# Optimization experiments

Measured on AMD Instinct MI355X. Metric: run time of the kernel, lower is better.

Reference implementation:

```python
import jax, jax.numpy as jnp
import numpy as np

IN_F = 4096
OUT_F = 4096
RANK = 16
ALPHA = 32
BLOCK = 64  # quantization blocksize along in_features
SCALING = ALPHA / RANK


def setup_inputs() -> dict:
    key = jax.random.key(0)
    k1, k2, k3, k4, k5, k6 = jax.random.split(key, 6)
    x = jax.random.normal(k1, (4, 2048, IN_F), dtype=jnp.float32)
    # int4 codes stored with +8 offset, values in [0, 16)
    q_codes = jax.random.randint(k2, (OUT_F, IN_F), 0, 16, dtype=jnp.int32)
    # per-(row, block) dequant scales
    scales = jax.random.uniform(k3, (OUT_F, IN_F // BLOCK), dtype=jnp.float32) * 0.02
    bias = jax.random.normal(k4, (OUT_F,), dtype=jnp.float32) * 0.02
    lora_A = jax.random.normal(k5, (RANK, IN_F), dtype=jnp.float32) * (1.0 / np.sqrt(IN_F))
    lora_B = jax.random.normal(k6, (OUT_F, RANK), dtype=jnp.float32) * 0.02
    return {"x": x, "q_codes": q_codes, "scales": scales, "bias": bias,
            "lora_A": lora_A, "lora_B": lora_B}


def _dequant(q_codes, scales):
    # [O, I] int4 codes (offset by 8) -> fp32 weight via blockwise scales
    O, I = q_codes.shape
    c = (q_codes.astype(jnp.float32) - 8.0).reshape(O, I // BLOCK, BLOCK)
    return (c * scales[:, :, None]).reshape(O, I)


def reference(x, q_codes, scales, bias, lora_A, lora_B):
    w = _dequant(q_codes, scales)                      # [O, I]
    base = jnp.einsum('bsi,oi->bso', x, w) + bias      # dequant GEMM + bias
    # LoRA branch: dropout(p=0) is identity; x @ (B@A).T == (x @ A.T) @ B.T
    lora = jnp.einsum('bsr,or->bso', jnp.einsum('bsi,ri->bsr', x, lora_A), lora_B)
    return base + lora * SCALING
```

## Files before the change

### kernel.cpp

```cpp
#include <hip/hip_runtime.h>
#include <hip/hip_bf16.h>

#define IN_F   4096
#define OUT_F  4096
#define RANK   16
#define M_TOK  8192
#define SCALING 2.0f

typedef __attribute__((ext_vector_type(8))) short short8;
typedef __attribute__((ext_vector_type(4))) float f32x4;
typedef __attribute__((ext_vector_type(4))) float fvec4;
typedef __attribute__((ext_vector_type(4))) int   ivec4;
typedef __attribute__((ext_vector_type(4))) unsigned int uvec4;

__global__ __launch_bounds__(256) void cvt_x(const float* __restrict__ x,
                                             __hip_bfloat16* __restrict__ xb) {
    const size_t nvec = (size_t)M_TOK * IN_F / 8;
    const size_t stride = (size_t)gridDim.x * 256;
    for (size_t idx = (size_t)blockIdx.x * 256 + threadIdx.x; idx < nvec; idx += stride) {
        const size_t i = idx * 8;
        fvec4 a = __builtin_nontemporal_load((const fvec4*)(x + i));
        fvec4 b = __builtin_nontemporal_load((const fvec4*)(x + i + 4));
        union { uvec4 u; __hip_bfloat16 h[8]; } p;
        p.h[0] = __float2bfloat16(a.x);
        p.h[1] = __float2bfloat16(a.y);
        p.h[2] = __float2bfloat16(a.z);
        p.h[3] = __float2bfloat16(a.w);
        p.h[4] = __float2bfloat16(b.x);
        p.h[5] = __float2bfloat16(b.y);
        p.h[6] = __float2bfloat16(b.z);
        p.h[7] = __float2bfloat16(b.w);
        *(uvec4*)(xb + i) = p.u;
    }
}

__global__ __launch_bounds__(256) void dequant_lora(const int* __restrict__ q,
                                                    const float* __restrict__ sc,
                                                    const float* __restrict__ lA,
                                                    const float* __restrict__ lB,
                                                    __hip_bfloat16* __restrict__ W) {
    const int tid = threadIdx.x;
    const int id  = blockIdx.x;
    const int c0  = (id & 3) * 1024 + tid * 4;
    const int o0  = (id >> 2) * 8;

    ivec4 qv[8];
#pragma unroll
    for (int oo = 0; oo < 8; ++oo)
        qv[oo] = __builtin_nontemporal_load(
            (const ivec4*)(q + (size_t)(o0 + oo) * IN_F + c0));

    float sv[8];
#pragma unroll
    for (int oo = 0; oo < 8; ++oo)
        sv[oo] = sc[(o0 + oo) * (IN_F / 64) + (c0 >> 6)];

    fvec4 a[RANK];
#pragma unroll
    for (int r = 0; r < RANK; ++r)
        a[r] = *(const fvec4*)(lA + (size_t)r * IN_F + c0);

#pragma unroll
    for (int oo = 0; oo < 8; ++oo) {
        const float* lbo = lB + (size_t)(o0 + oo) * RANK;
        float l0 = 0.f, l1 = 0.f, l2 = 0.f, l3 = 0.f;
#pragma unroll
        for (int r = 0; r < RANK; ++r) {
            const float br = lbo[r];
            l0 += br * a[r].x; l1 += br * a[r].y;
            l2 += br * a[r].z; l3 += br * a[r].w;
        }
        const float s = sv[oo];
        union { ushort4 u; __hip_bfloat16 h[4]; } p;
        p.h[0] = __float2bfloat16((float)(qv[oo].x - 8) * s + SCALING * l0);
        p.h[1] = __float2bfloat16((float)(qv[oo].y - 8) * s + SCALING * l1);
        p.h[2] = __float2bfloat16((float)(qv[oo].z - 8) * s + SCALING * l2);
        p.h[3] = __float2bfloat16((float)(qv[oo].w - 8) * s + SCALING * l3);
        *(ushort4*)(W + (size_t)(o0 + oo) * IN_F + c0) = p.u;
    }
}


__device__ __forceinline__ void load_lds16(const void* g, void* l) {
    __builtin_amdgcn_global_load_lds(
        (const __attribute__((address_space(1))) unsigned int*)g,
        (__attribute__((address_space(3))) unsigned int*)l, 16, 0, 0);
}

#define MFMA_BF16 __builtin_amdgcn_mfma_f32_16x16x32_bf16

__global__ __launch_bounds__(512, 2) void gemm256_8ph(const __hip_bfloat16* __restrict__ A,
                                                      const __hip_bfloat16* __restrict__ B,
                                                      const float* __restrict__ bias,
                                                      float* __restrict__ C) {
    extern __shared__ __align__(16) char lds[];

    const int tid  = threadIdx.x;
    const int lane = tid & 63;
    const int wave = tid >> 6;

    const int xcd = blockIdx.x & 7;
    const int w64 = blockIdx.x >> 3;
    const int tm  = (xcd >> 1) * 8 + (w64 >> 3);
    const int tn  = (xcd & 1) * 8 + (w64 & 7);

    const __hip_bfloat16* Ab = A + (size_t)tm * 256 * IN_F;
    const __hip_bfloat16* Bb = B + (size_t)tn * 256 * IN_F;

    const int    c0   = ((lane & 3) * 8) ^ ((lane >= 32) ? 16 : 0);
    const size_t off0 = (size_t)((wave >> 1) * 16 + (lane >> 2)) * IN_F
                      + (size_t)((wave & 1) * 32 + c0);

    const __hip_bfloat16* qA0 = Ab + off0;
    const __hip_bfloat16* qA1 = Ab + (size_t)128 * IN_F + off0;
    const __hip_bfloat16* qB0 = Bb + off0;
    const __hip_bfloat16* qB1 = Bb + (size_t)128 * IN_F + off0;

    const int flo = (lane & 15) * 64 + (((lane >> 4) * 16) ^ ((lane & 8) << 2));

    const int ah = wave >> 2;
    const int bh = (wave >> 1) & 1;
    const int bs = (wave & 1) * 4;

    const char* aRd[2] = { lds + ah * 16384 + flo,
                           lds + 65536 + ah * 16384 + flo };
    const char* bRd[2] = { lds + 32768 + bh * 16384 + bs * 2048 + flo,
                           lds + 65536 + 32768 + bh * 16384 + bs * 2048 + flo };

    const int wv1024 = wave * 1024;

#define STAGE2(ps, te, LO) do {                                             \
        const __hip_bfloat16* g_ = (ps) + (te);                             \
        load_lds16(g_,              lds + (LO) + wv1024);                   \
        load_lds16(g_ + 64 * IN_F,  lds + (LO) + 8192 + wv1024);            \
    } while (0)

    STAGE2(qB0, 0,  32768);
    STAGE2(qB1, 0,  49152);
    STAGE2(qA0, 0,  0);
    STAGE2(qA1, 0,  16384);
    STAGE2(qB0, 64, 65536 + 32768);
    STAGE2(qB1, 64, 65536 + 49152);
    asm volatile("s_waitcnt vmcnt(4)" ::: "memory");
    __builtin_amdgcn_s_barrier();

    short8 aF[4][2], bAf[2][2], bBf[2][2];
    f32x4 acc[8][4] = {};

#define TILE(T, CBI) do {                                                          \
        const int t1e = (((T) + 1) & 63) << 6;        \
        const int t2e = (((T) + 2) & 63) << 6;                                     \
                           \
        _Pragma("unroll")                                                          \
        for (int i = 0; i < 4; ++i)                                                \
            _Pragma("unroll")                                                      \
            for (int kk = 0; kk < 2; ++kk)                                         \
                aF[i][kk] = *(const short8*)(aRd[CBI] + (i * 2 + kk) * 1024);      \
        _Pragma("unroll")                                                          \
        for (int j = 0; j < 2; ++j)                                                \
            _Pragma("unroll")                                                      \
            for (int kk = 0; kk < 2; ++kk)                                         \
                bAf[j][kk] = *(const short8*)(bRd[CBI] + (j * 2 + kk) * 1024);     \
        STAGE2(qA0, t1e, ((CBI) ^ 1) * 65536);                                     \
        __builtin_amdgcn_s_barrier();                                              \
        __builtin_amdgcn_s_setprio(1);                                             \
        _Pragma("unroll")                                                          \
        for (int i = 0; i < 4; ++i)                                                \
            _Pragma("unroll")                                                      \
            for (int j = 0; j < 2; ++j)                                            \
                _Pragma("unroll")                                                  \
                for (int kk = 0; kk < 2; ++kk)                                     \
                    acc[i][j] = MFMA_BF16(aF[i][kk], bAf[j][kk], acc[i][j], 0,0,0);\
        __builtin_amdgcn_s_setprio(0);                                             \
        __builtin_amdgcn_s_barrier();                                              \
                           \
        _Pragma("unroll")                                                          \
        for (int j = 0; j < 2; ++j)                                                \
            _Pragma("unroll")                                                      \
            for (int kk = 0; kk < 2; ++kk)                                         \
                bBf[j][kk] = *(const short8*)(bRd[CBI] + 4096 + (j*2+kk) * 1024);  \
        STAGE2(qA1, t1e, ((CBI) ^ 1) * 65536 + 16384);                             \
        __builtin_amdgcn_s_barrier();                                              \
        __builtin_amdgcn_s_setprio(1);                                             \
        _Pragma("unroll")                                                          \
        for (int i = 0; i < 4; ++i)                                                \
            _Pragma("unroll")                                                      \
            for (int j = 0; j < 2; ++j)                                            \
                _Pragma("unroll")                                                  \
                for (int kk = 0; kk < 2; ++kk)                                     \
                    acc[i][2+j] = MFMA_BF16(aF[i][kk], bBf[j][kk], acc[i][2+j],0,0,0);\
        __builtin_amdgcn_s_setprio(0);                                             \
        __builtin_amdgcn_s_barrier();                                              \
                           \
        _Pragma("unroll")                                                          \
        for (int i = 0; i < 4; ++i)                                                \
            _Pragma("unroll")                                                      \
            for (int kk = 0; kk < 2; ++kk)                                         \
                aF[i][kk] = *(const short8*)(aRd[CBI] + 8192 + (i*2+kk) * 1024);   \
        STAGE2(qB0, t2e, (CBI) * 65536 + 32768);               \
        __builtin_amdgcn_s_barrier();                                              \
        __builtin_amdgcn_s_setprio(1);                                             \
        _Pragma("unroll")                                                          \
        for (int i = 0; i < 4; ++i)                                                \
            _Pragma("unroll")                                                      \
            for (int j = 0; j < 2; ++j)                                            \
                _Pragma("unroll")                                                  \
                for (int kk = 0; kk < 2; ++kk)                                     \
                    acc[4+i][2+j] = MFMA_BF16(aF[i][kk], bBf[j][kk], acc[4+i][2+j],0,0,0);\
        __builtin_amdgcn_s_setprio(0);                                             \
        __builtin_amdgcn_s_barrier();                                              \
                           \
        STAGE2(qB1, t2e, (CBI) * 65536 + 49152);                                   \
        asm volatile("s_waitcnt vmcnt(4)" ::: "memory");      \
        __builtin_amdgcn_s_barrier();                          \
        __builtin_amdgcn_s_setprio(1);                                             \
        _Pragma("unroll")                                                          \
        for (int i = 0; i < 4; ++i)                                                \
            _Pragma("unroll")                                                      \
            for (int j = 0; j < 2; ++j)                                            \
                _Pragma("unroll")                                                  \
                for (int kk = 0; kk < 2; ++kk)                                     \
                    acc[4+i][j] = MFMA_BF16(aF[i][kk], bAf[j][kk], acc[4+i][j],0,0,0);\
        __builtin_amdgcn_s_setprio(0);                                             \
        __builtin_amdgcn_s_barrier();                                              \
    } while (0)

    for (int tt = 0; tt < 32; ++tt) {
        TILE(2 * tt,     0);
        TILE(2 * tt + 1, 1);
    }
    asm volatile("s_waitcnt vmcnt(0)" ::: "memory");

    const int qd = lane >> 4;
    const int cl = lane & 15;
    const size_t m_base = (size_t)tm * 256 + (size_t)ah * 128;
    const int    n_base = tn * 256 + (wave & 3) * 64;
#pragma unroll
    for (int fn = 0; fn < 4; ++fn) {
        const int n = n_base + fn * 16 + cl;
        const float bv = bias[n];
#pragma unroll
        for (int fm = 0; fm < 8; ++fm) {
            const size_t m0 = m_base + fm * 16 + qd * 4;
#pragma unroll
            for (int r = 0; r < 4; ++r)
                __builtin_nontemporal_store(acc[fm][fn][r] + bv,
                                            &C[(m0 + r) * OUT_F + n]);
        }
    }
#undef STAGE2
#undef TILE
}

extern "C" void kernel_launch(void* const* d_in, const int* in_sizes, int n_in,
                              void* d_out, int out_size, void* d_ws, size_t ws_size,
                              hipStream_t stream) {
    const float* x    = (const float*)d_in[0];
    const int*   qc   = (const int*)d_in[1];
    const float* sc   = (const float*)d_in[2];
    const float* bias = (const float*)d_in[3];
    const float* lA   = (const float*)d_in[4];
    const float* lB   = (const float*)d_in[5];
    float* out = (float*)d_out;

    __hip_bfloat16* xb = (__hip_bfloat16*)d_ws;
    __hip_bfloat16* wb = xb + (size_t)M_TOK * IN_F;

    static bool attr_done = false;
    if (!attr_done) {
        (void)hipFuncSetAttribute((const void*)gemm256_8ph,
                                  hipFuncAttributeMaxDynamicSharedMemorySize, 131072);
        attr_done = true;
    }

    cvt_x<<<2048, 256, 0, stream>>>(x, xb);
    dequant_lora<<<2048, 256, 0, stream>>>(qc, sc, lA, lB, wb);
    gemm256_8ph<<<dim3(512), dim3(512), 131072, stream>>>(xb, wb, bias, out);
}
```

Measured before the change: 481.6 us.

## Switch GEMM core to 32x32x16 bf16 MFMA with matching LDS layout

Replaces the 16x16x32 MFMA tiling with 32x32x16 MFMA instructions, reorganising per-wave fragments into 2x2 blocks of 32x32 accumulators. The global-to-LDS staging layout and the LDS read addressing change to a plain 32-row layout without the previous XOR swizzle, and the epilogue is rewritten for the 32x32 output layout. The aim is fewer MFMA issues and fewer LDS fragment reads per tile. The cost is a risk of LDS bank conflicts now that the swizzle is gone.

New measurement: 505.7 us. 5.0% more time.

```diff
diff --git a/kernel.cpp b/kernel.cpp
--- a/kernel.cpp
+++ b/kernel.cpp
@@ -7,11 +7,12 @@
 #define M_TOK  8192
 #define SCALING 2.0f
 
-typedef __attribute__((ext_vector_type(8))) short short8;
-typedef __attribute__((ext_vector_type(4))) float f32x4;
-typedef __attribute__((ext_vector_type(4))) float fvec4;
-typedef __attribute__((ext_vector_type(4))) int   ivec4;
-typedef __attribute__((ext_vector_type(4))) unsigned int uvec4;
+typedef __attribute__((ext_vector_type(8)))  short short8;
+typedef __attribute__((ext_vector_type(4)))  float f32x4;
+typedef __attribute__((ext_vector_type(16))) float f32x16;
+typedef __attribute__((ext_vector_type(4)))  float fvec4;
+typedef __attribute__((ext_vector_type(4)))  int   ivec4;
+typedef __attribute__((ext_vector_type(4)))  unsigned int uvec4;
 
 __global__ __launch_bounds__(256) void cvt_x(const float* __restrict__ x,
                                              __hip_bfloat16* __restrict__ xb) {
@@ -87,7 +88,7 @@
         (__attribute__((address_space(3))) unsigned int*)l, 16, 0, 0);
 }
 
-#define MFMA_BF16 __builtin_amdgcn_mfma_f32_16x16x32_bf16
+#define MFMA32 __builtin_amdgcn_mfma_f32_32x32x16_bf16
 
 __global__ __launch_bounds__(512, 2) void gemm256_8ph(const __hip_bfloat16* __restrict__ A,
                                                       const __hip_bfloat16* __restrict__ B,
@@ -107,25 +108,23 @@
     const __hip_bfloat16* Ab = A + (size_t)tm * 256 * IN_F;
     const __hip_bfloat16* Bb = B + (size_t)tn * 256 * IN_F;
 
-    const int    c0   = ((lane & 3) * 8) ^ ((lane >= 32) ? 16 : 0);
-    const size_t off0 = (size_t)((wave >> 1) * 16 + (lane >> 2)) * IN_F
-                      + (size_t)((wave & 1) * 32 + c0);
+    const size_t off0 = (size_t)((wave >> 2) * 32 + (lane >> 1)) * IN_F
+                      + (size_t)((wave & 3) * 16 + (lane & 1) * 8);
 
     const __hip_bfloat16* qA0 = Ab + off0;
     const __hip_bfloat16* qA1 = Ab + (size_t)128 * IN_F + off0;
     const __hip_bfloat16* qB0 = Bb + off0;
     const __hip_bfloat16* qB1 = Bb + (size_t)128 * IN_F + off0;
 
-    const int flo = (lane & 15) * 64 + (((lane >> 4) * 16) ^ ((lane & 8) << 2));
+    const int lrd = (lane & 31) * 32 + (lane >> 5) * 16;
 
     const int ah = wave >> 2;
     const int bh = (wave >> 1) & 1;
-    const int bs = (wave & 1) * 4;
-
-    const char* aRd[2] = { lds + ah * 16384 + flo,
-                           lds + 65536 + ah * 16384 + flo };
-    const char* bRd[2] = { lds + 32768 + bh * 16384 + bs * 2048 + flo,
-                           lds + 65536 + 32768 + bh * 16384 + bs * 2048 + flo };
+
+    const char* aRd[2] = { lds + ah * 16384 + lrd,
+                           lds + 65536 + ah * 16384 + lrd };
+    const char* bRd[2] = { lds + 32768 + bh * 16384 + (wave & 1) * 8192 + lrd,
+                           lds + 65536 + 32768 + bh * 16384 + (wave & 1) * 8192 + lrd };
 
     const int wv1024 = wave * 1024;
 
@@ -144,83 +143,71 @@
     asm volatile("s_waitcnt vmcnt(4)" ::: "memory");
     __builtin_amdgcn_s_barrier();
 
-    short8 aF[4][2], bAf[2][2], bBf[2][2];
-    f32x4 acc[8][4] = {};
+    short8 aF[2][4], bA[4], bB[4];
+    f32x16 acc[4][2] = {};
 
 #define TILE(T, CBI) do {                                                          \
         const int t1e = (((T) + 1) & 63) << 6;        \
         const int t2e = (((T) + 2) & 63) << 6;                                     \
-                           \
-        _Pragma("unroll")                                                          \
-        for (int i = 0; i < 4; ++i)                                                \
+                          \
+        _Pragma("unroll")                                                          \
+        for (int i = 0; i < 2; ++i)                                                \
             _Pragma("unroll")                                                      \
-            for (int kk = 0; kk < 2; ++kk)                                         \
-                aF[i][kk] = *(const short8*)(aRd[CBI] + (i * 2 + kk) * 1024);      \
-        _Pragma("unroll")                                                          \
-        for (int j = 0; j < 2; ++j)                                                \
+            for (int ks = 0; ks < 4; ++ks)                                         \
+                aF[i][ks] = *(const short8*)(aRd[CBI] + (i * 4 + ks) * 1024);      \
+        _Pragma("unroll")                                                          \
+        for (int ks = 0; ks < 4; ++ks)                                             \
+            bA[ks] = *(const short8*)(bRd[CBI] + ks * 1024);                       \
+        STAGE2(qA0, t1e, ((CBI) ^ 1) * 65536);                                     \
+        __builtin_amdgcn_s_barrier();                                              \
+        __builtin_amdgcn_s_setprio(1);                                             \
+        _Pragma("unroll")                                                          \
+        for (int ks = 0; ks < 4; ++ks) {                                           \
+            acc[0][0] = MFMA32(aF[0][ks], bA[ks], acc[0][0], 0, 0, 0);             \
+            acc[1][0] = MFMA32(aF[1][ks], bA[ks], acc[1][0], 0, 0, 0);             \
+        }                                                                          \
+        __builtin_amdgcn_s_setprio(0);                                             \
+        __builtin_amdgcn_s_barrier();                                              \
+                          \
+        _Pragma("unroll")                                                          \
+        for (int ks = 0; ks < 4; ++ks)                                             \
+            bB[ks] = *(const short8*)(bRd[CBI] + 4096 + ks * 1024);                \
+        STAGE2(qA1, t1e, ((CBI) ^ 1) * 65536 + 16384);                             \
+        __builtin_amdgcn_s_barrier();                                              \
+        __builtin_amdgcn_s_setprio(1);                                             \
+        _Pragma("unroll")                                                          \
+        for (int ks = 0; ks < 4; ++ks) {                                           \
+            acc[0][1] = MFMA32(aF[0][ks], bB[ks], acc[0][1], 0, 0, 0);             \
+            acc[1][1] = MFMA32(aF[1][ks], bB[ks], acc[1][1], 0, 0, 0);             \
+        }                                                                          \
+        __builtin_amdgcn_s_setprio(0);                                             \
+        __builtin_amdgcn_s_barrier();                                              \
+                          \
+        _Pragma("unroll")                                                          \
+        for (int i = 0; i < 2; ++i)                                                \
             _Pragma("unroll")                                                      \
-            for (int kk = 0; kk < 2; ++kk)                                         \
-                bAf[j][kk] = *(const short8*)(bRd[CBI] + (j * 2 + kk) * 1024);     \
-        STAGE2(qA0, t1e, ((CBI) ^ 1) * 65536);                                     \
-        __builtin_amdgcn_s_barrier();                                              \
-        __builtin_amdgcn_s_setprio(1);                                             \
-        _Pragma("unroll")                                                          \
-        for (int i = 0; i < 4; ++i)                                                \
-            _Pragma("unroll")                                                      \
-            for (int j = 0; j < 2; ++j)                                            \
-                _Pragma("unroll")                                                  \
-                for (int kk = 0; kk < 2; ++kk)                                     \
-                    acc[i][j] = MFMA_BF16(aF[i][kk], bAf[j][kk], acc[i][j], 0,0,0);\
-        __builtin_amdgcn_s_setprio(0);                                             \
-        __builtin_amdgcn_s_barrier();                                              \
-                           \
-        _Pragma("unroll")                                                          \
-        for (int j = 0; j < 2; ++j)                                                \
-            _Pragma("unroll")                                                      \
-            for (int kk = 0; kk < 2; ++kk)                                         \
-                bBf[j][kk] = *(const short8*)(bRd[CBI] + 4096 + (j*2+kk) * 1024);  \
-        STAGE2(qA1, t1e, ((CBI) ^ 1) * 65536 + 16384);                             \
-        __builtin_amdgcn_s_barrier();                                              \
-        __builtin_amdgcn_s_setprio(1);                                             \
-        _Pragma("unroll")                                                          \
-        for (int i = 0; i < 4; ++i)                                                \
-            _Pragma("unroll")                                                      \
-            for (int j = 0; j < 2; ++j)                                            \
-                _Pragma("unroll")                                                  \
-                for (int kk = 0; kk < 2; ++kk)                                     \
-                    acc[i][2+j] = MFMA_BF16(aF[i][kk], bBf[j][kk], acc[i][2+j],0,0,0);\
-        __builtin_amdgcn_s_setprio(0);                                             \
-        __builtin_amdgcn_s_barrier();                                              \
-                           \
-        _Pragma("unroll")                                                          \
-        for (int i = 0; i < 4; ++i)                                                \
-            _Pragma("unroll")                                                      \
-            for (int kk = 0; kk < 2; ++kk)                                         \
-                aF[i][kk] = *(const short8*)(aRd[CBI] + 8192 + (i*2+kk) * 1024);   \
-        STAGE2(qB0, t2e, (CBI) * 65536 + 32768);               \
-        __builtin_amdgcn_s_barrier();                                              \
-        __builtin_amdgcn_s_setprio(1);                                             \
-        _Pragma("unroll")                                                          \
-        for (int i = 0; i < 4; ++i)                                                \
-            _Pragma("unroll")                                                      \
-            for (int j = 0; j < 2; ++j)                                            \
-                _Pragma("unroll")                                                  \
-                for (int kk = 0; kk < 2; ++kk)                                     \
-                    acc[4+i][2+j] = MFMA_BF16(aF[i][kk], bBf[j][kk], acc[4+i][2+j],0,0,0);\
-        __builtin_amdgcn_s_setprio(0);                                             \
-        __builtin_amdgcn_s_barrier();                                              \
-                           \
+            for (int ks = 0; ks < 4; ++ks)                                         \
+                aF[i][ks] = *(const short8*)(aRd[CBI] + 8192 + (i * 4 + ks) * 1024);\
+        STAGE2(qB0, t2e, (CBI) * 65536 + 32768);         \
+        __builtin_amdgcn_s_barrier();                                              \
+        __builtin_amdgcn_s_setprio(1);                                             \
+        _Pragma("unroll")                                                          \
+        for (int ks = 0; ks < 4; ++ks) {                                           \
+            acc[2][1] = MFMA32(aF[0][ks], bB[ks], acc[2][1], 0, 0, 0);             \
+            acc[3][1] = MFMA32(aF[1][ks], bB[ks], acc[3][1], 0, 0, 0);             \
+        }                                                                          \
+        __builtin_amdgcn_s_setprio(0);                                             \
+        __builtin_amdgcn_s_barrier();                                              \
+                          \
         STAGE2(qB1, t2e, (CBI) * 65536 + 49152);                                   \
         asm volatile("s_waitcnt vmcnt(4)" ::: "memory");      \
         __builtin_amdgcn_s_barrier();                          \
         __builtin_amdgcn_s_setprio(1);                                             \
         _Pragma("unroll")                                                          \
-        for (int i = 0; i < 4; ++i)                                                \
-            _Pragma("unroll")                                                      \
-            for (int j = 0; j < 2; ++j)                                            \
-                _Pragma("unroll")                                                  \
-                for (int kk = 0; kk < 2; ++kk)                                     \
-                    acc[4+i][j] = MFMA_BF16(aF[i][kk], bAf[j][kk], acc[4+i][j],0,0,0);\
+        for (int ks = 0; ks < 4; ++ks) {                                           \
+            acc[2][0] = MFMA32(aF[0][ks], bA[ks], acc[2][0], 0, 0, 0);             \
+            acc[3][0] = MFMA32(aF[1][ks], bA[ks], acc[3][0], 0, 0, 0);             \
+        }                                                                          \
         __builtin_amdgcn_s_setprio(0);                                             \
         __builtin_amdgcn_s_barrier();                                              \
     } while (0)
@@ -231,21 +218,24 @@
     }
     asm volatile("s_waitcnt vmcnt(0)" ::: "memory");
 
-    const int qd = lane >> 4;
-    const int cl = lane & 15;
-    const size_t m_base = (size_t)tm * 256 + (size_t)ah * 128;
+    const int cl = lane & 31;
+    const int hi = lane >> 5;
+    const size_t m_base = (size_t)tm * 256 + (size_t)ah * 128 + hi * 4;
     const int    n_base = tn * 256 + (wave & 3) * 64;
 #pragma unroll
-    for (int fn = 0; fn < 4; ++fn) {
-        const int n = n_base + fn * 16 + cl;
+    for (int cb = 0; cb < 2; ++cb) {
+        const int n = n_base + cb * 32 + cl;
         const float bv = bias[n];
 #pragma unroll
-        for (int fm = 0; fm < 8; ++fm) {
-            const size_t m0 = m_base + fm * 16 + qd * 4;
-#pragma unroll
-            for (int r = 0; r < 4; ++r)
-                __builtin_nontemporal_store(acc[fm][fn][r] + bv,
-                                            &C[(m0 + r) * OUT_F + n]);
+        for (int rb = 0; rb < 4; ++rb) {
+#pragma unroll
+            for (int g = 0; g < 4; ++g) {
+                const size_t m0 = m_base + rb * 32 + g * 8;
+#pragma unroll
+                for (int rr = 0; rr < 4; ++rr)
+                    __builtin_nontemporal_store(acc[rb][cb][g * 4 + rr] + bv,
+                                                &C[(m0 + rr) * OUT_F + n]);
+            }
         }
     }
 #undef STAGE2
```
